# Kernel tuning notes

Measured on AMD Instinct MI355X. Metric: run time of the kernel, lower is better.

The kernel has to match this reference:

```python
import jax, jax.numpy as jnp
import numpy as np

B, I, A_IN = 32, 32, 16     # batch, input capsules, input atoms
OD, OA = 10, 16             # output_dim (classes), output_atoms
H, W = 12, 12               # spatial grid
NUM_ROUTING = 3


def _squash(t):
    # squash over atom dim (axis=2): x/|x| * |x|^2/(1+|x|^2) = x*|x|/(1+|x|^2)
    norm = jnp.linalg.norm(t, axis=2, keepdims=True)
    return t * norm / (1.0 + norm * norm)


def setup_inputs() -> dict:
    key = jax.random.key(0)
    k1, k2 = jax.random.split(key)
    x = jax.random.normal(k1, (B, I, A_IN, H, W), dtype=jnp.float32)
    # torch weight: (I, A_IN, OD*OA, 1, 1), init N(0, 0.1)
    weight = 0.1 * jax.random.normal(k2, (I, A_IN, OD * OA), dtype=jnp.float32)
    # torch bias: (OD, OA, 1, 1), init const 0.1
    bias = jnp.full((OD, OA, 1, 1), 0.1, dtype=jnp.float32)
    return {"x": x, "weight": weight, "bias": bias}


def reference(x, weight, bias):
    # votes: sum over input atoms -> [B, I, OD*OA, H, W] -> [B, I, OD, OA, H, W]
    votes = jnp.einsum("biahw,iak->bikhw", x, weight)
    votes = votes.reshape(B, I, OD, OA, H, W)
    biases = jnp.broadcast_to(bias, (OD, OA, H, W))

    # Dynamic routing. In the original, logits carry no gradient (built from
    # .data), so intermediate iterations are fully stop-gradient.
    votes_sg = jax.lax.stop_gradient(votes)
    logits = jnp.zeros((B, I, OD, H, W), dtype=votes.dtype)
    activation = None
    for i in range(NUM_ROUTING):
        route = jax.nn.softmax(logits, axis=2)  # softmax over output_dim
        v = votes if i == NUM_ROUTING - 1 else votes_sg
        preact = jnp.einsum("bidhw,bidahw->bdahw", route, v) + biases
        activation = _squash(preact)  # [B, OD, OA, H, W]
        if i < NUM_ROUTING - 1:
            # agreement (dot over atoms) updates logits
            logits = logits + jnp.einsum(
                "bidahw,bdahw->bidhw", votes_sg, jax.lax.stop_gradient(activation)
            )
    return activation
```

## Files before the change

### kernel.cpp

```cpp
#include <hip/hip_runtime.h>
#include <math.h>

#define NB 32
#define NI 32
#define NA 16
#define NOD 10
#define NOA 16
#define NK (NOD*NOA)
#define NHW 144
#define NROUT 3
#define P 2
#define NTHREADS 512
#define SVLD (NK + 1)

__global__ __launch_bounds__(NTHREADS)
void capsule_routing_kernel(const float* __restrict__ x,
                            const float* __restrict__ weight,
                            const float* __restrict__ bias,
                            float* __restrict__ out)
{
    __shared__ float sx[NI][NA][P];
    __shared__ float sv[P * NI * SVLD];
    __shared__ float slog[P][NI][NOD];
    __shared__ float srt[P][NI][NOD];
    __shared__ float sact[P][NOD][NOA + 1];

    const int bk  = blockIdx.x;
    const int b   = bk / (NHW / P);
    const int hw0 = (bk % (NHW / P)) * P;
    const int tid = threadIdx.x;

#define SV(p, i, k) sv[((p) * NI + (i)) * SVLD + (k)]

    if (tid < NI * NA) {
        const int i = tid >> 4;
        const int a = tid & (NA - 1);
        const float2 v = *reinterpret_cast<const float2*>(
            x + (size_t)((b * NI + i) * NA + a) * NHW + hw0);
        sx[i][a][0] = v.x;
        sx[i][a][1] = v.y;
    }
    {
        float* lf = &slog[0][0][0];
        for (int j = tid; j < P * NI * NOD; j += NTHREADS) lf[j] = 0.0f;
    }
    __syncthreads();

    for (int j = tid; j < NI * NK; j += NTHREADS) {
        const int i = j / NK;
        const int k = j - i * NK;
        const float* wp = weight + (size_t)i * NA * NK + k;
        float acc0 = 0.0f, acc1 = 0.0f;
#pragma unroll
        for (int a = 0; a < NA; ++a) {
            const float wv = wp[a * NK];
            acc0 = fmaf(sx[i][a][0], wv, acc0);
            acc1 = fmaf(sx[i][a][1], wv, acc1);
        }
        SV(0, i, k) = acc0;
        SV(1, i, k) = acc1;
    }
    __syncthreads();

    for (int it = 0; it < NROUT; ++it) {
        if (tid < P * NI) {
            const int p = tid >> 5;
            const int i = tid & 31;
            float m = slog[p][i][0];
#pragma unroll
            for (int od = 1; od < NOD; ++od) m = fmaxf(m, slog[p][i][od]);
            float s = 0.0f;
            float e[NOD];
#pragma unroll
            for (int od = 0; od < NOD; ++od) {
                e[od] = __expf(slog[p][i][od] - m);
                s += e[od];
            }
            const float inv = 1.0f / s;
#pragma unroll
            for (int od = 0; od < NOD; ++od) srt[p][i][od] = e[od] * inv;
        }
        __syncthreads();

        if (tid < P * NK) {
            const int p  = tid / NK;
            const int k  = tid - p * NK;
            const int od = k >> 4;
            const int oa = k & (NOA - 1);
            float acc = bias[k];
#pragma unroll 8
            for (int i = 0; i < NI; ++i)
                acc = fmaf(srt[p][i][od], SV(p, i, k), acc);
            float ss = acc * acc;
#pragma unroll
            for (int m = 1; m < NOA; m <<= 1)
                ss += __shfl_xor(ss, m, NOA);
            const float scale = sqrtf(ss) / (1.0f + ss);
            sact[p][od][oa] = acc * scale;
        }
        __syncthreads();

        if (it < NROUT - 1) {
            for (int j = tid; j < P * NI * NOD; j += NTHREADS) {
                const int p  = j / (NI * NOD);
                const int r  = j - p * (NI * NOD);
                const int od = r >> 5;
                const int i  = r & 31;
                float acc = 0.0f;
#pragma unroll
                for (int oa = 0; oa < NOA; ++oa)
                    acc = fmaf(SV(p, i, od * NOA + oa), sact[p][od][oa], acc);
                slog[p][i][od] += acc;
            }
            __syncthreads();
        }
    }

    __syncthreads();
    if (tid < NK) {
        const int od = tid >> 4;
        const int oa = tid & (NOA - 1);
        const float2 v = make_float2(sact[0][od][oa], sact[1][od][oa]);
        *reinterpret_cast<float2*>(out + (size_t)(b * NK + tid) * NHW + hw0) = v;
    }
}

extern "C" void kernel_launch(void* const* d_in, const int* in_sizes, int n_in,
                              void* d_out, int out_size, void* d_ws, size_t ws_size,
                              hipStream_t stream) {
    const float* x      = (const float*)d_in[0];
    const float* weight = (const float*)d_in[1];
    const float* bias   = (const float*)d_in[2];
    float* out          = (float*)d_out;

    const int nblocks = NB * (NHW / P);
    capsule_routing_kernel<<<nblocks, NTHREADS, 0, stream>>>(x, weight, bias, out);
}
```

Measured before the change: 52.91 us.

## Store votes in shared memory as bf16 and vectorize weight loads

Stores the per-block votes tile in LDS as bf16 instead of fp32, halving shared-memory footprint, which may allow more resident blocks. Vote computation now loads weights as float4 and writes packed ushort4. The agreement step reads 16 bf16 values with two 128-bit loads. This trades accuracy, since votes are rounded to bf16 before routing, for lower LDS usage and bandwidth.

```diff
diff --git a/kernel.cpp b/kernel.cpp
--- a/kernel.cpp
+++ b/kernel.cpp
@@ -6,12 +6,27 @@
 #define NA 16
 #define NOD 10
 #define NOA 16
-#define NK (NOD*NOA)
+#define NK 160
 #define NHW 144
 #define NROUT 3
 #define P 2
 #define NTHREADS 512
-#define SVLD (NK + 1)
+#define SVLD 168
+
+__device__ __forceinline__ unsigned short f2bf(float f) {
+    unsigned b = __builtin_bit_cast(unsigned, f);
+    b += 0x7fffu + ((b >> 16) & 1u);
+    return (unsigned short)(b >> 16);
+}
+__device__ __forceinline__ float bf2f(unsigned short u) {
+    return __builtin_bit_cast(float, (unsigned)u << 16);
+}
+__device__ __forceinline__ float bf_lo(unsigned d) {
+    return __builtin_bit_cast(float, d << 16);
+}
+__device__ __forceinline__ float bf_hi(unsigned d) {
+    return __builtin_bit_cast(float, d & 0xffff0000u);
+}
 
 __global__ __launch_bounds__(NTHREADS)
 void capsule_routing_kernel(const float* __restrict__ x,
@@ -20,17 +35,17 @@
                             float* __restrict__ out)
 {
     __shared__ float sx[NI][NA][P];
-    __shared__ float sv[P * NI * SVLD];
+    __shared__ unsigned short sv[P * NI * SVLD];
     __shared__ float slog[P][NI][NOD];
     __shared__ float srt[P][NI][NOD];
-    __shared__ float sact[P][NOD][NOA + 1];
+    __shared__ float sact[P][NOD][NOA];
 
     const int bk  = blockIdx.x;
     const int b   = bk / (NHW / P);
     const int hw0 = (bk % (NHW / P)) * P;
     const int tid = threadIdx.x;
 
-#define SV(p, i, k) sv[((p) * NI + (i)) * SVLD + (k)]
+#define SVIDX(p, i, k) (((p) * NI + (i)) * SVLD + (k))
 
     if (tid < NI * NA) {
         const int i = tid >> 4;
@@ -46,19 +61,26 @@
     }
     __syncthreads();
 
-    for (int j = tid; j < NI * NK; j += NTHREADS) {
-        const int i = j / NK;
-        const int k = j - i * NK;
-        const float* wp = weight + (size_t)i * NA * NK + k;
-        float acc0 = 0.0f, acc1 = 0.0f;
+    for (int j = tid; j < NI * (NK / 4); j += NTHREADS) {
+        const int i  = j / (NK / 4);
+        const int k0 = (j - i * (NK / 4)) * 4;
+        const float4* wp = reinterpret_cast<const float4*>(
+            weight + (size_t)i * NA * NK + k0);
+        float4 a0 = make_float4(0.f, 0.f, 0.f, 0.f);
+        float4 a1 = make_float4(0.f, 0.f, 0.f, 0.f);
 #pragma unroll
         for (int a = 0; a < NA; ++a) {
-            const float wv = wp[a * NK];
-            acc0 = fmaf(sx[i][a][0], wv, acc0);
-            acc1 = fmaf(sx[i][a][1], wv, acc1);
+            const float4 w4 = wp[a * (NK / 4)];
+            const float2 xa = *reinterpret_cast<const float2*>(&sx[i][a][0]);
+            a0.x = fmaf(xa.x, w4.x, a0.x); a0.y = fmaf(xa.x, w4.y, a0.y);
+            a0.z = fmaf(xa.x, w4.z, a0.z); a0.w = fmaf(xa.x, w4.w, a0.w);
+            a1.x = fmaf(xa.y, w4.x, a1.x); a1.y = fmaf(xa.y, w4.y, a1.y);
+            a1.z = fmaf(xa.y, w4.z, a1.z); a1.w = fmaf(xa.y, w4.w, a1.w);
         }
-        SV(0, i, k) = acc0;
-        SV(1, i, k) = acc1;
+        ushort4 s0 = make_ushort4(f2bf(a0.x), f2bf(a0.y), f2bf(a0.z), f2bf(a0.w));
+        ushort4 s1 = make_ushort4(f2bf(a1.x), f2bf(a1.y), f2bf(a1.z), f2bf(a1.w));
+        *reinterpret_cast<ushort4*>(&sv[SVIDX(0, i, k0)]) = s0;
+        *reinterpret_cast<ushort4*>(&sv[SVIDX(1, i, k0)]) = s1;
     }
     __syncthreads();
 
@@ -69,8 +91,8 @@
             float m = slog[p][i][0];
 #pragma unroll
             for (int od = 1; od < NOD; ++od) m = fmaxf(m, slog[p][i][od]);
+            float e[NOD];
             float s = 0.0f;
-            float e[NOD];
 #pragma unroll
             for (int od = 0; od < NOD; ++od) {
                 e[od] = __expf(slog[p][i][od] - m);
@@ -88,9 +110,10 @@
             const int od = k >> 4;
             const int oa = k & (NOA - 1);
             float acc = bias[k];
-#pragma unroll 8
+            const unsigned short* svp = &sv[SVIDX(p, 0, k)];
+#pragma unroll
             for (int i = 0; i < NI; ++i)
-                acc = fmaf(srt[p][i][od], SV(p, i, k), acc);
+                acc = fmaf(srt[p][i][od], bf2f(svp[i * SVLD]), acc);
             float ss = acc * acc;
 #pragma unroll
             for (int m = 1; m < NOA; m <<= 1)
@@ -106,10 +129,28 @@
                 const int r  = j - p * (NI * NOD);
                 const int od = r >> 5;
                 const int i  = r & 31;
-                float acc = 0.0f;
-#pragma unroll
-                for (int oa = 0; oa < NOA; ++oa)
-                    acc = fmaf(SV(p, i, od * NOA + oa), sact[p][od][oa], acc);
+                const uint4 d0 = *reinterpret_cast<const uint4*>(
+                    &sv[SVIDX(p, i, od * NOA)]);
+                const uint4 d1 = *reinterpret_cast<const uint4*>(
+                    &sv[SVIDX(p, i, od * NOA + 8)]);
+                const float* ap = &sact[p][od][0];
+                float acc;
+                acc  = bf_lo(d0.x) * ap[0];
+                acc = fmaf(bf_hi(d0.x), ap[1], acc);
+                acc = fmaf(bf_lo(d0.y), ap[2], acc);
+                acc = fmaf(bf_hi(d0.y), ap[3], acc);
+                acc = fmaf(bf_lo(d0.z), ap[4], acc);
+                acc = fmaf(bf_hi(d0.z), ap[5], acc);
+                acc = fmaf(bf_lo(d0.w), ap[6], acc);
+                acc = fmaf(bf_hi(d0.w), ap[7], acc);
+                acc = fmaf(bf_lo(d1.x), ap[8], acc);
+                acc = fmaf(bf_hi(d1.x), ap[9], acc);
+                acc = fmaf(bf_lo(d1.y), ap[10], acc);
+                acc = fmaf(bf_hi(d1.y), ap[11], acc);
+                acc = fmaf(bf_lo(d1.z), ap[12], acc);
+                acc = fmaf(bf_hi(d1.z), ap[13], acc);
+                acc = fmaf(bf_lo(d1.w), ap[14], acc);
+                acc = fmaf(bf_hi(d1.w), ap[15], acc);
                 slog[p][i][od] += acc;
             }
             __syncthreads();
```

Result: faster. 47.92 us (-9.4%).
